# Kernel tuning notes

Hardware: AMD Instinct MI355X
Metric: run time of the kernel (lower is better)

Reference implementation:

```python
import jax, jax.numpy as jnp
import numpy as np

K = 21        # classes
SAMPLES = 8   # 'allNums' normalizer in cal_iou
BETA = 1.0
EPS = 1e-10


def _batched_hists(pred, gt):
    """pred, gt: [B, N] int. Returns (inter, area_out, area_tgt) each [B, K].
    Replaces the per-sample torch.histc loop with one fused scatter-add pass."""
    B, N = gt.shape
    base = (jnp.arange(B, dtype=jnp.int32)[:, None] * K)  # [B,1]
    hit = (pred == gt).astype(jnp.float32).reshape(-1)
    idx_gt = (base + gt).reshape(-1)
    idx_pr = (base + pred).reshape(-1)
    inter = jnp.zeros(B * K, jnp.float32).at[idx_gt].add(hit).reshape(B, K)
    a_tgt = jnp.zeros(B * K, jnp.float32).at[idx_gt].add(1.0).reshape(B, K)
    a_out = jnp.zeros(B * K, jnp.float32).at[idx_pr].add(1.0).reshape(B, K)
    return inter, a_out, a_tgt


def setup_inputs() -> dict:
    key = jax.random.key(0)
    k1, k2 = jax.random.split(key)
    pr = jax.random.normal(k1, (8, K, 512, 512), dtype=jnp.float32)
    gt = jax.random.randint(k2, (8, 512, 512), 0, K, dtype=jnp.int32)
    return {"pr": pr, "gt": gt}


def reference(pr, gt):
    B = pr.shape[0]
    # argmax(softmax(pr)) == argmax(pr)
    pred = jnp.argmax(pr, axis=1).astype(jnp.int32)          # [B, H, W]
    predf = pred.reshape(B, -1)
    gtf = gt.reshape(B, -1)

    inter, a_out, a_tgt = _batched_hists(predf, gtf)          # [B, K] each
    union = a_out + a_tgt - inter
    dice_class = (2.0 * inter / (union + inter + EPS)).sum(0) / SAMPLES  # [K]
    weight = jax.lax.stop_gradient(1.0 - dice_class)          # detached, like torch

    # weighted cross-entropy, reduction='mean' (torch semantics: / sum of weights)
    logp = jax.nn.log_softmax(pr, axis=1)                     # [B, K, H, W]
    logp_gt = jnp.take_along_axis(logp, gt[:, None], axis=1)[:, 0]  # [B, H, W]
    w_pix = weight[gt]                                        # [B, H, W]
    celoss = -(w_pix * logp_gt).sum() / w_pix.sum()

    dice_oppo = jnp.mean(weight)
    return BETA * dice_oppo + celoss
```

## Files before the change

kernel.cpp:

```cpp
#include <hip/hip_runtime.h>

#define KCLS 21
#define HW (512 * 512)
#define BATCH 8
#define NBLK 1024
#define BLKSZ 256


__global__ __launch_bounds__(BLKSZ) void dicece_histo(
    const float* __restrict__ pr, const int* __restrict__ gt,
    unsigned int* __restrict__ ws_inter, unsigned int* __restrict__ ws_aout,
    unsigned int* __restrict__ ws_atgt, float* __restrict__ ws_S)
{
    __shared__ unsigned int s_inter[KCLS], s_aout[KCLS], s_atgt[KCLS];
    __shared__ float s_S[KCLS];
    const int t = threadIdx.x;
    if (t < KCLS) { s_inter[t] = 0u; s_aout[t] = 0u; s_atgt[t] = 0u; s_S[t] = 0.f; }
    __syncthreads();

    const int blocks_per_img = NBLK / BATCH;
    const int b = blockIdx.x / blocks_per_img;
    const int chunk = blockIdx.x - b * blocks_per_img;
    const int PIXB = HW / blocks_per_img;
    const int pix0 = chunk * PIXB;

    const float* __restrict__ pb = pr + (size_t)b * KCLS * HW;
    const int*   __restrict__ gb = gt + (size_t)b * HW;

    #pragma unroll
    for (int it = 0; it < PIXB / (BLKSZ * 4); ++it) {
        const int pix = pix0 + (it * BLKSZ + t) * 4;

        float x[KCLS][4];
        #pragma unroll
        for (int k = 0; k < KCLS; ++k) {
            *reinterpret_cast<float4*>(&x[k][0]) =
                *reinterpret_cast<const float4*>(pb + (size_t)k * HW + pix);
        }
        int g[4];
        *reinterpret_cast<int4*>(&g[0]) = *reinterpret_cast<const int4*>(gb + pix);

        #pragma unroll
        for (int j = 0; j < 4; ++j) {
            float m = x[0][j];
            int am = 0;
            #pragma unroll
            for (int k = 1; k < KCLS; ++k) {
                if (x[k][j] > m) { m = x[k][j]; am = k; }
            }
            float s = 0.f;
            #pragma unroll
            for (int k = 0; k < KCLS; ++k) s += __expf(x[k][j] - m);
            const int gj = g[j];
            float xg = x[0][j];
            #pragma unroll
            for (int k = 1; k < KCLS; ++k) xg = (k == gj) ? x[k][j] : xg;
            const float logp = xg - m - __logf(s);

            atomicAdd(&s_atgt[gj], 1u);
            atomicAdd(&s_aout[am], 1u);
            if (am == gj) atomicAdd(&s_inter[gj], 1u);
            atomicAdd(&s_S[gj], logp);
        }
    }
    __syncthreads();
    if (t < KCLS) {
        atomicAdd(&ws_inter[b * KCLS + t], s_inter[t]);
        atomicAdd(&ws_aout [b * KCLS + t], s_aout[t]);
        atomicAdd(&ws_atgt [b * KCLS + t], s_atgt[t]);
        atomicAdd(&ws_S[t], s_S[t]);
    }
}

__global__ void dicece_final(
    const unsigned int* __restrict__ ws_inter, const unsigned int* __restrict__ ws_aout,
    const unsigned int* __restrict__ ws_atgt, const float* __restrict__ ws_S,
    float* __restrict__ out)
{
    const int k = threadIdx.x;
    float w = 0.f, Nk = 0.f, Sk = 0.f;
    if (k < KCLS) {
        float dsum = 0.f;
        unsigned int nk = 0u;
        #pragma unroll
        for (int b = 0; b < BATCH; ++b) {
            const float inter = (float)ws_inter[b * KCLS + k];
            const float ao    = (float)ws_aout [b * KCLS + k];
            const float at    = (float)ws_atgt [b * KCLS + k];
            nk += ws_atgt[b * KCLS + k];
            dsum += 2.f * inter / (ao + at + 1e-10f);
        }
        w  = 1.f - dsum * 0.125f;
        Nk = (float)nk;
        Sk = ws_S[k];
    }
    float num = w * Sk, den = w * Nk, wsum = w;
    #pragma unroll
    for (int off = 32; off > 0; off >>= 1) {
        num  += __shfl_down(num, off);
        den  += __shfl_down(den, off);
        wsum += __shfl_down(wsum, off);
    }
    if (k == 0) out[0] = wsum / (float)KCLS - num / den;
}

extern "C" void kernel_launch(void* const* d_in, const int* in_sizes, int n_in,
                              void* d_out, int out_size, void* d_ws, size_t ws_size,
                              hipStream_t stream) {
    const float* pr = (const float*)d_in[0];
    const int*   gt = (const int*)d_in[1];
    float* out = (float*)d_out;

    unsigned int* ws_inter = (unsigned int*)d_ws;
    unsigned int* ws_aout  = ws_inter + BATCH * KCLS;
    unsigned int* ws_atgt  = ws_aout  + BATCH * KCLS;
    float*        ws_S     = (float*)(ws_atgt + BATCH * KCLS);

    hipMemsetAsync(d_ws, 0, (size_t)(3 * BATCH * KCLS + KCLS) * sizeof(float), stream);
    dicece_histo<<<NBLK, BLKSZ, 0, stream>>>(pr, gt, ws_inter, ws_aout, ws_atgt, ws_S);
    dicece_final<<<1, 64, 0, stream>>>(ws_inter, ws_aout, ws_atgt, ws_S, out);
}
```

Before: 48.17 us.

## Fuse final reduction via last-block pattern and pack histogram atomics into 64-bit

Merges the finalize kernel into the histogram kernel using a done-counter so the last block computes the loss, removing one launch. Per-pixel shared atomics are cut from four to two by packing the intersection flag, target count and a fixed-point -logp into one 64-bit add, and histograms are privatized per wave to reduce contention. Grid doubles to 2048 blocks with 2 pixels per thread, a non-unrolled loop and a launch-bounds occupancy hint. Fixed-point quantization of logp adds small rounding error and relies on per-block sums fitting in 32 bits.

```diff
diff --git a/kernel.cpp b/kernel.cpp
--- a/kernel.cpp
+++ b/kernel.cpp
@@ -3,51 +3,52 @@
 #define KCLS 21
 #define HW (512 * 512)
 #define BATCH 8
-#define NBLK 1024
+#define NBLK 2048
 #define BLKSZ 256
+#define NWAVE 4
+#define BPI (NBLK / BATCH)
+#define PIXB (HW / BPI)
+#define ITERS (PIXB / (BLKSZ * 2))
 
 
-__global__ __launch_bounds__(BLKSZ) void dicece_histo(
+__global__ __launch_bounds__(BLKSZ, 5) void dicece_fused(
     const float* __restrict__ pr, const int* __restrict__ gt,
-    unsigned int* __restrict__ ws_inter, unsigned int* __restrict__ ws_aout,
-    unsigned int* __restrict__ ws_atgt, float* __restrict__ ws_S)
+    unsigned long long* __restrict__ ws_ti, unsigned int* __restrict__ ws_aout,
+    float* __restrict__ ws_S, unsigned int* __restrict__ ws_done,
+    float* __restrict__ out)
 {
-    __shared__ unsigned int s_inter[KCLS], s_aout[KCLS], s_atgt[KCLS];
-    __shared__ float s_S[KCLS];
+    __shared__ unsigned long long s_gj[NWAVE][KCLS];
+    __shared__ unsigned int s_out[NWAVE][KCLS];
+    __shared__ unsigned int s_last;
     const int t = threadIdx.x;
-    if (t < KCLS) { s_inter[t] = 0u; s_aout[t] = 0u; s_atgt[t] = 0u; s_S[t] = 0.f; }
+    const int w = t >> 6;
+    if (t < NWAVE * KCLS) { (&s_gj[0][0])[t] = 0ull; (&s_out[0][0])[t] = 0u; }
+    if (t == 0) s_last = 0u;
     __syncthreads();
 
-    const int blocks_per_img = NBLK / BATCH;
-    const int b = blockIdx.x / blocks_per_img;
-    const int chunk = blockIdx.x - b * blocks_per_img;
-    const int PIXB = HW / blocks_per_img;
+    const int b = blockIdx.x / BPI;
+    const int chunk = blockIdx.x - b * BPI;
     const int pix0 = chunk * PIXB;
-
     const float* __restrict__ pb = pr + (size_t)b * KCLS * HW;
     const int*   __restrict__ gb = gt + (size_t)b * HW;
 
-    #pragma unroll
-    for (int it = 0; it < PIXB / (BLKSZ * 4); ++it) {
-        const int pix = pix0 + (it * BLKSZ + t) * 4;
+    #pragma unroll 1
+    for (int it = 0; it < ITERS; ++it) {
+        const int pix = pix0 + (it * BLKSZ + t) * 2;
 
-        float x[KCLS][4];
+        float x[KCLS][2];
         #pragma unroll
-        for (int k = 0; k < KCLS; ++k) {
-            *reinterpret_cast<float4*>(&x[k][0]) =
-                *reinterpret_cast<const float4*>(pb + (size_t)k * HW + pix);
-        }
-        int g[4];
-        *reinterpret_cast<int4*>(&g[0]) = *reinterpret_cast<const int4*>(gb + pix);
+        for (int k = 0; k < KCLS; ++k)
+            *reinterpret_cast<float2*>(&x[k][0]) =
+                *reinterpret_cast<const float2*>(pb + (size_t)k * HW + pix);
+        int g[2];
+        *reinterpret_cast<int2*>(&g[0]) = *reinterpret_cast<const int2*>(gb + pix);
 
         #pragma unroll
-        for (int j = 0; j < 4; ++j) {
-            float m = x[0][j];
-            int am = 0;
+        for (int j = 0; j < 2; ++j) {
+            float m = x[0][j]; int am = 0;
             #pragma unroll
-            for (int k = 1; k < KCLS; ++k) {
-                if (x[k][j] > m) { m = x[k][j]; am = k; }
-            }
+            for (int k = 1; k < KCLS; ++k) if (x[k][j] > m) { m = x[k][j]; am = k; }
             float s = 0.f;
             #pragma unroll
             for (int k = 0; k < KCLS; ++k) s += __expf(x[k][j] - m);
@@ -55,53 +56,63 @@
             float xg = x[0][j];
             #pragma unroll
             for (int k = 1; k < KCLS; ++k) xg = (k == gj) ? x[k][j] : xg;
-            const float logp = xg - m - __logf(s);
-
-            atomicAdd(&s_atgt[gj], 1u);
-            atomicAdd(&s_aout[am], 1u);
-            if (am == gj) atomicAdd(&s_inter[gj], 1u);
-            atomicAdd(&s_S[gj], logp);
+            const float mag = (m - xg) + __logf(s);
+            const unsigned int fx = (unsigned int)(mag * 65536.f + 0.5f);
+            const unsigned long long pk =
+                ((unsigned long long)(am == gj) << 48) | (1ull << 32) |
+                (unsigned long long)fx;
+            atomicAdd(&s_gj[w][gj], pk);
+            atomicAdd(&s_out[w][am], 1u);
         }
     }
     __syncthreads();
+
     if (t < KCLS) {
-        atomicAdd(&ws_inter[b * KCLS + t], s_inter[t]);
-        atomicAdd(&ws_aout [b * KCLS + t], s_aout[t]);
-        atomicAdd(&ws_atgt [b * KCLS + t], s_atgt[t]);
-        atomicAdd(&ws_S[t], s_S[t]);
+        unsigned long long acc = 0ull; unsigned int ao = 0u;
+        #pragma unroll
+        for (int ww = 0; ww < NWAVE; ++ww) { acc += s_gj[ww][t]; ao += s_out[ww][t]; }
+        const unsigned int fx  = (unsigned int)(acc & 0xFFFFFFFFull);
+        const unsigned int tgt = (unsigned int)((acc >> 32) & 0xFFFFull);
+        const unsigned int itr = (unsigned int)(acc >> 48);
+        atomicAdd(&ws_ti[b * KCLS + t], ((unsigned long long)tgt << 32) | itr);
+        atomicAdd(&ws_aout[b * KCLS + t], ao);
+        atomicAdd(&ws_S[b * KCLS + t], (float)fx * (1.f / 65536.f));
     }
-}
+    __syncthreads();
 
-__global__ void dicece_final(
-    const unsigned int* __restrict__ ws_inter, const unsigned int* __restrict__ ws_aout,
-    const unsigned int* __restrict__ ws_atgt, const float* __restrict__ ws_S,
-    float* __restrict__ out)
-{
-    const int k = threadIdx.x;
-    float w = 0.f, Nk = 0.f, Sk = 0.f;
-    if (k < KCLS) {
-        float dsum = 0.f;
-        unsigned int nk = 0u;
+    if (t == 0) {
+        __threadfence();
+        const unsigned int r = atomicAdd(ws_done, 1u);
+        s_last = (r == NBLK - 1) ? 1u : 0u;
+    }
+    __syncthreads();
+    if (s_last == 0u || t >= 64) return;
+
+    float wgt = 0.f, Nk = 0.f, Sk = 0.f;
+    if (t < KCLS) {
+        float dsum = 0.f; unsigned int nk = 0u;
         #pragma unroll
-        for (int b = 0; b < BATCH; ++b) {
-            const float inter = (float)ws_inter[b * KCLS + k];
-            const float ao    = (float)ws_aout [b * KCLS + k];
-            const float at    = (float)ws_atgt [b * KCLS + k];
-            nk += ws_atgt[b * KCLS + k];
-            dsum += 2.f * inter / (ao + at + 1e-10f);
+        for (int bb = 0; bb < BATCH; ++bb) {
+            const unsigned long long ti = __hip_atomic_load(&ws_ti[bb * KCLS + t], __ATOMIC_RELAXED, __HIP_MEMORY_SCOPE_AGENT);
+            const unsigned int ao       = __hip_atomic_load(&ws_aout[bb * KCLS + t], __ATOMIC_RELAXED, __HIP_MEMORY_SCOPE_AGENT);
+            const float S               = __hip_atomic_load(&ws_S[bb * KCLS + t], __ATOMIC_RELAXED, __HIP_MEMORY_SCOPE_AGENT);
+            const unsigned int itr = (unsigned int)(ti & 0xFFFFFFFFull);
+            const unsigned int tgt = (unsigned int)(ti >> 32);
+            nk += tgt;
+            dsum += 2.f * (float)itr / ((float)ao + (float)tgt + 1e-10f);
+            Sk += S;
         }
-        w  = 1.f - dsum * 0.125f;
+        wgt = 1.f - dsum * 0.125f;
         Nk = (float)nk;
-        Sk = ws_S[k];
     }
-    float num = w * Sk, den = w * Nk, wsum = w;
+    float num = wgt * Sk, den = wgt * Nk, wsum = wgt;
     #pragma unroll
     for (int off = 32; off > 0; off >>= 1) {
-        num  += __shfl_down(num, off);
-        den  += __shfl_down(den, off);
+        num += __shfl_down(num, off);
+        den += __shfl_down(den, off);
         wsum += __shfl_down(wsum, off);
     }
-    if (k == 0) out[0] = wsum / (float)KCLS - num / den;
+    if (t == 0) out[0] = wsum * (1.f / (float)KCLS) + num / den;
 }
 
 extern "C" void kernel_launch(void* const* d_in, const int* in_sizes, int n_in,
@@ -111,12 +122,12 @@
     const int*   gt = (const int*)d_in[1];
     float* out = (float*)d_out;
 
-    unsigned int* ws_inter = (unsigned int*)d_ws;
-    unsigned int* ws_aout  = ws_inter + BATCH * KCLS;
-    unsigned int* ws_atgt  = ws_aout  + BATCH * KCLS;
-    float*        ws_S     = (float*)(ws_atgt + BATCH * KCLS);
+    unsigned long long* ws_ti   = (unsigned long long*)d_ws;
+    unsigned int*       ws_aout = (unsigned int*)(ws_ti + BATCH * KCLS);
+    float*              ws_S    = (float*)(ws_aout + BATCH * KCLS);
+    unsigned int*       ws_done = (unsigned int*)(ws_S + BATCH * KCLS);
 
-    hipMemsetAsync(d_ws, 0, (size_t)(3 * BATCH * KCLS + KCLS) * sizeof(float), stream);
-    dicece_histo<<<NBLK, BLKSZ, 0, stream>>>(pr, gt, ws_inter, ws_aout, ws_atgt, ws_S);
-    dicece_final<<<1, 64, 0, stream>>>(ws_inter, ws_aout, ws_atgt, ws_S, out);
+    const size_t zbytes = (size_t)(BATCH * KCLS) * (8 + 4 + 4) + 4;
+    hipMemsetAsync(d_ws, 0, zbytes, stream);
+    dicece_fused<<<NBLK, BLKSZ, 0, stream>>>(pr, gt, ws_ti, ws_aout, ws_S, ws_done, out);
 }
```

Result: slower. 101.4 us (+110.5%).
